# Optimization experiments

Measured on AMD Instinct MI355X. Metric: run time of the kernel, lower is better.

## Reference

```python
import jax, jax.numpy as jnp
import numpy as np

D_MODEL = 1024
STATE_DIM = 128


def setup_inputs() -> dict:
    key = jax.random.key(0)
    ks = jax.random.split(key, 8)
    B, T, D, N = 8, 4096, D_MODEL, STATE_DIM
    u = jax.random.normal(ks[0], (B, T, D), dtype=jnp.float32)
    h0 = jnp.zeros((B, N), dtype=jnp.float32)
    log_A = jax.random.normal(ks[1], (N,), dtype=jnp.float32) * 0.1 - 1.0
    B_w = jax.random.normal(ks[2], (N, D), dtype=jnp.float32) / np.sqrt(D)
    B_b = jax.random.normal(ks[3], (N,), dtype=jnp.float32) * 0.01
    C_w = jax.random.normal(ks[4], (D, N), dtype=jnp.float32) / np.sqrt(N)
    C_b = jax.random.normal(ks[5], (D,), dtype=jnp.float32) * 0.01
    D_param = jnp.ones((D,), dtype=jnp.float32) * 0.1
    log_dt = jax.random.normal(ks[6], (N,), dtype=jnp.float32) * 0.1 - 2.0
    return {"u": u, "h0": h0, "log_A": log_A, "B_w": B_w, "B_b": B_b,
            "C_w": C_w, "C_b": C_b, "D_param": D_param, "log_dt": log_dt}


def reference(u, h0, log_A, B_w, B_b, C_w, C_b, D_param, log_dt):
    # u: [B, T, D], h0: [B, N]
    dt = jnp.minimum(jnp.exp(log_dt), 1.0)          # [N]
    A = -jnp.exp(log_A)                             # [N]
    A_bar = jnp.exp(A * dt)                         # [N]
    # B_bar * u, precomputed for all timesteps: [B, T, N]
    Bu = (jnp.einsum('btd,nd->btn', u, B_w) + B_b) * dt

    def step(h, bu_t):
        h = A_bar * h + bu_t                        # [B, N]
        return h, h

    # scan over time: Bu transposed to [T, B, N]
    _, hs = jax.lax.scan(step, h0, jnp.swapaxes(Bu, 0, 1))
    hs = jnp.swapaxes(hs, 0, 1)                     # [B, T, N]
    # y = C h + c_bias + D * u
    y = jnp.einsum('btn,dn->btd', hs, C_w) + C_b + D_param * u
    return y
```

## Files before the change

### kernel.cpp

```cpp
#include <hip/hip_runtime.h>

#define B_SZ 8
#define T_SZ 4096
#define D_SZ 1024
#define N_SZ 128
#define M_SZ (B_SZ*T_SZ)
#define C1 32
#define NC1 (T_SZ/C1)
#define C2 64
#define NC2 (T_SZ/C2)

typedef __attribute__((ext_vector_type(8))) __bf16 bf16x8;
typedef __attribute__((ext_vector_type(4))) float f32x4;
typedef __attribute__((ext_vector_type(4))) unsigned int u32x4;
typedef __attribute__((ext_vector_type(4))) float fvec4;

static __device__ __forceinline__ unsigned short f2bf(float f){
  union { float f; unsigned int u; } v; v.f = f;
  unsigned int r = v.u + 0x7fffu + ((v.u >> 16) & 1u);
  return (unsigned short)(r >> 16);
}

static __device__ __forceinline__ float bf2f(unsigned short s){
  union { unsigned int u; float f; } v; v.u = ((unsigned)s) << 16;
  return v.f;
}

static __device__ __forceinline__ void cp16(const void* g, void* l){
  __builtin_amdgcn_global_load_lds(
      (const __attribute__((address_space(1))) void*)g,
      (__attribute__((address_space(3))) void*)l, 16, 0, 0);
}

static __device__ __forceinline__ f32x4 zero4(){
  f32x4 v = {0.f, 0.f, 0.f, 0.f};
  return v;
}

static __device__ __forceinline__ bf16x8 pack8(fvec4 a, fvec4 b){
  bf16x8 v;
  v[0]=(__bf16)a.x; v[1]=(__bf16)a.y; v[2]=(__bf16)a.z; v[3]=(__bf16)a.w;
  v[4]=(__bf16)b.x; v[5]=(__bf16)b.y; v[6]=(__bf16)b.z; v[7]=(__bf16)b.w;
  return v;
}

__global__ __launch_bounds__(256) void k_conv(const float* __restrict__ Bw,
                                              const float* __restrict__ Cw,
                                              unsigned short* __restrict__ bw,
                                              unsigned short* __restrict__ cw){
  int t = blockIdx.x*256 + threadIdx.x;
  {
    int n = t >> 10, k = t & 1023;
    int c = k >> 6, kk = k & 63;
    unsigned byte = (unsigned)c*16384u + (unsigned)n*128u
                  + (unsigned)((kk*2) ^ ((n&7)<<4));
    bw[byte>>1] = f2bf(Bw[n*1024 + k]);
  }
  {
    int d = t >> 7, k = t & 127;
    int c = d >> 7, dd = d & 127;
    unsigned byte = (unsigned)c*32768u + (unsigned)dd*256u
                  + (unsigned)((k*2) ^ ((dd&15)<<4));
    cw[byte>>1] = f2bf(Cw[d*128 + k]);
  }
}

__global__ __launch_bounds__(256, 4) void k_gemm1c(const float* __restrict__ u,
                                                   const unsigned short* __restrict__ bw,
                                                   const float* __restrict__ Bb,
                                                   const float* __restrict__ logA,
                                                   const float* __restrict__ logdt,
                                                   unsigned short* __restrict__ Bu_bf,
                                                   float* __restrict__ carry){
  __shared__ __align__(16) char smem[20480];
  unsigned short* lA = (unsigned short*)smem;
  unsigned short* lB = (unsigned short*)(smem + 4096);
  float*          BuT = (float*)smem;
  const int tid  = threadIdx.x;
  const int lane = tid & 63;
  const int wave = tid >> 6;
  const int bc   = blockIdx.x;
  const int m0   = bc * 32;
  const int l15  = lane & 15;
  const int lhi  = lane >> 4;
  const int rt   = (wave & 1) * 16;
  const int ct0  = (wave >> 1) * 4;

  f32x4 acc[4];
  #pragma unroll
  for (int i=0;i<4;++i) acc[i] = zero4();

  for (int kc=0; kc<16; ++kc){
    #pragma unroll
    for (int rep=0; rep<4; ++rep){
      const char* g = (const char*)bw + kc*16384 + rep*4096 + tid*16;
      cp16(g, (char*)lB + rep*4096 + tid*16);
    }
    {
      int row = tid >> 3, ks = tid & 7;
      const float* src = u + (size_t)(m0+row)*1024 + kc*64 + ks*8;
      fvec4 f0 = *(const fvec4*)src;
      fvec4 f1 = *(const fvec4*)(src+4);
      unsigned byte = (unsigned)row*128u + (unsigned)((ks*16) ^ ((row&7)<<4));
      *(bf16x8*)((char*)lA + byte) = pack8(f0, f1);
    }
    __syncthreads();
    #pragma unroll
    for (int k0=0; k0<64; k0+=32){
      int arow = rt + l15;
      int ak = k0 + lhi*8;
      bf16x8 af = *(const bf16x8*)((const char*)lA + arow*128 + ((ak*2) ^ ((arow&7)<<4)));
      #pragma unroll
      for (int j=0;j<4;++j){
        int bn = (ct0+j)*16 + l15;
        bf16x8 bfv = *(const bf16x8*)((const char*)lB + bn*128 + ((ak*2) ^ ((bn&7)<<4)));
        acc[j] = __builtin_amdgcn_mfma_f32_16x16x32_bf16(af, bfv, acc[j], 0, 0, 0);
      }
    }
    __builtin_amdgcn_s_barrier();
    __builtin_amdgcn_sched_barrier(0);
  }

  #pragma unroll
  for (int j=0;j<4;++j){
    int n = (ct0+j)*16 + l15;
    float dt = fminf(__expf(logdt[n]), 1.f);
    float bb = Bb[n];
    #pragma unroll
    for (int r=0;r<4;++r){
      int ml = rt + lhi*4 + r;
      BuT[ml*128 + n] = (acc[j][r] + bb) * dt;
    }
  }
  __syncthreads();

  #pragma unroll
  for (int i=0;i<2;++i){
    int q = i*256 + tid;
    const float* s = BuT + q*8;
    fvec4 a = *(const fvec4*)s;
    fvec4 b = *(const fvec4*)(s+4);
    u32x4 p;
    p.x = (unsigned)f2bf(a.x) | ((unsigned)f2bf(a.y)<<16);
    p.y = (unsigned)f2bf(a.z) | ((unsigned)f2bf(a.w)<<16);
    p.z = (unsigned)f2bf(b.x) | ((unsigned)f2bf(b.y)<<16);
    p.w = (unsigned)f2bf(b.z) | ((unsigned)f2bf(b.w)<<16);
    *(u32x4*)((char*)Bu_bf + (size_t)bc*8192 + (size_t)q*16) = p;
  }

  if (tid < 128){
    int n = tid;
    float dt = fminf(__expf(logdt[n]), 1.f);
    float Ab = __expf(-__expf(logA[n]) * dt);
    float h = 0.f;
    #pragma unroll 8
    for (int j=0;j<C1;++j) h = fmaf(Ab, h, BuT[j*128 + n]);
    carry[(size_t)bc*128 + n] = h;
  }
}

__global__ __launch_bounds__(256) void k_gemm2s(const unsigned short* __restrict__ Bu_bf,
                                                const float* __restrict__ carry,
                                                const unsigned short* __restrict__ cw,
                                                const float* __restrict__ u,
                                                const float* __restrict__ h0,
                                                const float* __restrict__ Cb,
                                                const float* __restrict__ Dp,
                                                const float* __restrict__ logA,
                                                const float* __restrict__ logdt,
                                                float* __restrict__ y){
  __shared__ __align__(16) unsigned short BuT[64*128];
  __shared__ __align__(16) unsigned short hsT[64*128];
  __shared__ __align__(16) unsigned short cwT[128*128];
  const int tid = threadIdx.x, lane = tid & 63, wave = tid >> 6;
  const int bc = blockIdx.x;
  const int m0 = bc * 64;
  const int l15 = lane & 15, lhi = lane >> 4;

  #pragma unroll
  for (int i=0;i<4;++i){
    int off = i*4096 + tid*16;
    cp16((const char*)Bu_bf + (size_t)bc*16384 + off, (char*)BuT + off);
  }
  #pragma unroll
  for (int i=0;i<8;++i){
    int off = i*4096 + tid*16;
    cp16((const char*)cw + off, (char*)cwT + off);
  }

  float hreg = 0.f, Ab = 0.f;
  if (tid < 128){
    int n = tid;
    int b = bc >> 6;
    int c32 = (bc & 63) * 2;
    float dt = fminf(__expf(logdt[n]), 1.f);
    float Ad = -__expf(logA[n]) * dt;
    Ab = __expf(Ad);
    float AL = __expf(Ad * (float)C1);
    float h = h0[b*128 + n];
    const float* cp = carry + (size_t)b*NC1*128 + n;
    for (int g=0; g<8; ++g){
      if (g*16 >= c32) break;
      float cbuf[16];
      #pragma unroll
      for (int i=0;i<16;++i) cbuf[i] = cp[(size_t)(g*16+i)*128];
      #pragma unroll
      for (int i=0;i<16;++i){
        int idx = g*16 + i;
        h = (idx < c32) ? fmaf(AL, h, cbuf[i]) : h;
      }
    }
    hreg = h;
  }
  __syncthreads();

  if (tid < 128){
    int n = tid;
    float h = hreg;
    #pragma unroll 8
    for (int j=0;j<C2;++j){
      h = fmaf(Ab, h, bf2f(BuT[j*128 + n]));
      unsigned byte = (unsigned)j*256u + (unsigned)((n*2) ^ ((j&15)<<4));
      *(unsigned short*)((char*)hsT + byte) = f2bf(h);
    }
  }
  __syncthreads();

  for (int d=0; d<8; ++d){
    f32x4 acc[8];
    #pragma unroll
    for (int i=0;i<8;++i) acc[i] = zero4();

    #pragma unroll
    for (int k0=0;k0<128;k0+=32){
      int arow = wave*16 + l15;
      int ak = k0 + lhi*8;
      bf16x8 af = *(const bf16x8*)((const char*)hsT + arow*256 + ((ak*2) ^ ((arow&15)<<4)));
      #pragma unroll
      for (int ct=0;ct<8;++ct){
        int dn = ct*16 + l15;
        bf16x8 bfv = *(const bf16x8*)((const char*)cwT + dn*256 + ((ak*2) ^ ((dn&15)<<4)));
        acc[ct] = __builtin_amdgcn_mfma_f32_16x16x32_bf16(af, bfv, acc[ct], 0, 0, 0);
      }
    }
    __builtin_amdgcn_s_barrier();
    __builtin_amdgcn_sched_barrier(0);

    if (d < 7){
      #pragma unroll
      for (int i=0;i<8;++i){
        int off = (wave*8 + i)*1024 + lane*16;
        cp16((const char*)cw + (size_t)(d+1)*32768 + off, (char*)cwT + off);
      }
    }

    const int d0 = d*128;
    #pragma unroll
    for (int ct=0;ct<8;++ct){
      int dc = d0 + ct*16 + l15;
      float cb = Cb[dc], dp = Dp[dc];
      #pragma unroll
      for (int r=0;r<4;++r){
        int m = m0 + wave*16 + lhi*4 + r;
        size_t off = (size_t)m*1024 + dc;
        y[off] = acc[ct][r] + cb + dp*u[off];
      }
    }
    asm volatile("s_waitcnt vmcnt(32)" ::: "memory");
    __builtin_amdgcn_s_barrier();
    __builtin_amdgcn_sched_barrier(0);
  }
}

extern "C" void kernel_launch(void* const* d_in, const int* in_sizes, int n_in,
                              void* d_out, int out_size, void* d_ws, size_t ws_size,
                              hipStream_t stream){
  (void)in_sizes; (void)n_in; (void)out_size; (void)ws_size;
  const float* u     = (const float*)d_in[0];
  const float* h0    = (const float*)d_in[1];
  const float* logA  = (const float*)d_in[2];
  const float* Bw    = (const float*)d_in[3];
  const float* Bb    = (const float*)d_in[4];
  const float* Cw    = (const float*)d_in[5];
  const float* Cb    = (const float*)d_in[6];
  const float* Dp    = (const float*)d_in[7];
  const float* logdt = (const float*)d_in[8];
  float* y = (float*)d_out;

  char* ws = (char*)d_ws;
  unsigned short* Bu_bf = (unsigned short*)(ws);
  float*          carry = (float*)(ws + 8388608);
  unsigned short* bw    = (unsigned short*)(ws + 8912896);
  unsigned short* cw    = (unsigned short*)(ws + 9175040);

  k_conv  <<<dim3(512),  dim3(256), 0, stream>>>(Bw, Cw, bw, cw);
  k_gemm1c<<<dim3(1024), dim3(256), 0, stream>>>(u, bw, Bb, logA, logdt, Bu_bf, carry);
  k_gemm2s<<<dim3(512),  dim3(256), 0, stream>>>(Bu_bf, carry, cw, u, h0, Cb, Dp,
                                                 logA, logdt, y);
}
```

Baseline: 86.66 us.

## Split scan from second GEMM and keep C weights in registers

Moves the carry propagation and intra-chunk scan into a separate k_scan kernel that writes bf16 hidden states, already laid out in the swizzled order, to workspace. The second GEMM is reorganised so each block owns one 128-wide D slice, holds that slice of C_w in registers for the whole block, and loops over 8 M-tiles with double-buffered async loads of the hidden states. This removes the serial scan from the GEMM kernel's critical path and stops each block from reloading all of C_w. In exchange it adds a kernel launch, an extra global round trip for hs, and heavy register use (launch_bounds 256,2).

```diff
diff --git a/kernel.cpp b/kernel.cpp
--- a/kernel.cpp
+++ b/kernel.cpp
@@ -117,8 +117,7 @@
         acc[j] = __builtin_amdgcn_mfma_f32_16x16x32_bf16(af, bfv, acc[j], 0, 0, 0);
       }
     }
-    __builtin_amdgcn_s_barrier();
-    __builtin_amdgcn_sched_barrier(0);
+    __syncthreads();
   }
 
   #pragma unroll
@@ -159,113 +158,126 @@
   }
 }
 
-__global__ __launch_bounds__(256) void k_gemm2s(const unsigned short* __restrict__ Bu_bf,
-                                                const float* __restrict__ carry,
-                                                const unsigned short* __restrict__ cw,
-                                                const float* __restrict__ u,
-                                                const float* __restrict__ h0,
-                                                const float* __restrict__ Cb,
-                                                const float* __restrict__ Dp,
-                                                const float* __restrict__ logA,
-                                                const float* __restrict__ logdt,
-                                                float* __restrict__ y){
-  __shared__ __align__(16) unsigned short BuT[64*128];
-  __shared__ __align__(16) unsigned short hsT[64*128];
-  __shared__ __align__(16) unsigned short cwT[128*128];
+__global__ __launch_bounds__(128) void k_scan(const unsigned short* __restrict__ Bu_bf,
+                                              const float* __restrict__ carry,
+                                              const float* __restrict__ h0,
+                                              const float* __restrict__ logA,
+                                              const float* __restrict__ logdt,
+                                              unsigned short* __restrict__ hs){
+  const int bc = blockIdx.x;
+  const int n  = threadIdx.x;
+  const int b  = bc >> 6;
+  const int c32 = (bc & 63) * 2;
+  float dt = fminf(__expf(logdt[n]), 1.f);
+  float Ad = -__expf(logA[n]) * dt;
+  float Ab = __expf(Ad);
+  float AL = __expf(Ad * (float)C1);
+  float h = h0[b*128 + n];
+  const float* cp = carry + (size_t)b*NC1*128 + n;
+  for (int g=0; g<8; ++g){
+    if (g*16 >= c32) break;
+    float cbuf[16];
+    #pragma unroll
+    for (int i=0;i<16;++i) cbuf[i] = cp[(size_t)(g*16+i)*128];
+    #pragma unroll
+    for (int i=0;i<16;++i){
+      int idx = g*16 + i;
+      h = (idx < c32) ? fmaf(AL, h, cbuf[i]) : h;
+    }
+  }
+  const unsigned short* bp = Bu_bf + (size_t)bc*C2*128 + n;
+  char* hbase = (char*)hs + (size_t)bc*16384;
+  #pragma unroll 8
+  for (int j=0;j<C2;++j){
+    h = fmaf(Ab, h, bf2f(bp[(size_t)j*128]));
+    unsigned byte = (unsigned)j*256u + (unsigned)((n*2) ^ ((j&15)<<4));
+    *(unsigned short*)(hbase + byte) = f2bf(h);
+  }
+}
+
+__global__ __launch_bounds__(256, 2) void k_gemm2(const unsigned short* __restrict__ hs,
+                                                  const unsigned short* __restrict__ cw,
+                                                  const float* __restrict__ u,
+                                                  const float* __restrict__ Cb,
+                                                  const float* __restrict__ Dp,
+                                                  float* __restrict__ y){
+  __shared__ __align__(16) unsigned short hsA[2][64*128];
   const int tid = threadIdx.x, lane = tid & 63, wave = tid >> 6;
-  const int bc = blockIdx.x;
-  const int m0 = bc * 64;
+  const int bid = blockIdx.x;
+  const int mg = bid & 63;
+  const int d  = bid >> 6;
   const int l15 = lane & 15, lhi = lane >> 4;
+  const int d0 = d*128;
 
   #pragma unroll
   for (int i=0;i<4;++i){
     int off = i*4096 + tid*16;
-    cp16((const char*)Bu_bf + (size_t)bc*16384 + off, (char*)BuT + off);
-  }
-  #pragma unroll
-  for (int i=0;i<8;++i){
-    int off = i*4096 + tid*16;
-    cp16((const char*)cw + off, (char*)cwT + off);
-  }
-
-  float hreg = 0.f, Ab = 0.f;
-  if (tid < 128){
-    int n = tid;
-    int b = bc >> 6;
-    int c32 = (bc & 63) * 2;
-    float dt = fminf(__expf(logdt[n]), 1.f);
-    float Ad = -__expf(logA[n]) * dt;
-    Ab = __expf(Ad);
-    float AL = __expf(Ad * (float)C1);
-    float h = h0[b*128 + n];
-    const float* cp = carry + (size_t)b*NC1*128 + n;
-    for (int g=0; g<8; ++g){
-      if (g*16 >= c32) break;
-      float cbuf[16];
-      #pragma unroll
-      for (int i=0;i<16;++i) cbuf[i] = cp[(size_t)(g*16+i)*128];
-      #pragma unroll
-      for (int i=0;i<16;++i){
-        int idx = g*16 + i;
-        h = (idx < c32) ? fmaf(AL, h, cbuf[i]) : h;
-      }
-    }
-    hreg = h;
-  }
-  __syncthreads();
-
-  if (tid < 128){
-    int n = tid;
-    float h = hreg;
-    #pragma unroll 8
-    for (int j=0;j<C2;++j){
-      h = fmaf(Ab, h, bf2f(BuT[j*128 + n]));
-      unsigned byte = (unsigned)j*256u + (unsigned)((n*2) ^ ((j&15)<<4));
-      *(unsigned short*)((char*)hsT + byte) = f2bf(h);
-    }
-  }
-  __syncthreads();
-
-  for (int d=0; d<8; ++d){
-    f32x4 acc[8];
-    #pragma unroll
-    for (int i=0;i<8;++i) acc[i] = zero4();
-
-    #pragma unroll
-    for (int k0=0;k0<128;k0+=32){
-      int arow = wave*16 + l15;
-      int ak = k0 + lhi*8;
-      bf16x8 af = *(const bf16x8*)((const char*)hsT + arow*256 + ((ak*2) ^ ((arow&15)<<4)));
+    cp16((const char*)hs + (size_t)(mg*8)*16384 + off, (char*)hsA[0] + off);
+  }
+
+  bf16x8 bfr[4][8];
+  {
+    const char* cwd = (const char*)cw + (size_t)d*32768;
+    #pragma unroll
+    for (int k0i=0;k0i<4;++k0i){
+      int ak = k0i*32 + lhi*8;
       #pragma unroll
       for (int ct=0;ct<8;++ct){
         int dn = ct*16 + l15;
-        bf16x8 bfv = *(const bf16x8*)((const char*)cwT + dn*256 + ((ak*2) ^ ((dn&15)<<4)));
-        acc[ct] = __builtin_amdgcn_mfma_f32_16x16x32_bf16(af, bfv, acc[ct], 0, 0, 0);
-      }
-    }
-    __builtin_amdgcn_s_barrier();
-    __builtin_amdgcn_sched_barrier(0);
-
-    if (d < 7){
-      #pragma unroll
-      for (int i=0;i<8;++i){
-        int off = (wave*8 + i)*1024 + lane*16;
-        cp16((const char*)cw + (size_t)(d+1)*32768 + off, (char*)cwT + off);
-      }
-    }
-
-    const int d0 = d*128;
+        bfr[k0i][ct] = *(const bf16x8*)(cwd + dn*256 + ((ak*2) ^ ((dn&15)<<4)));
+      }
+    }
+  }
+  float cbv[8], dpv[8];
+  #pragma unroll
+  for (int ct=0;ct<8;++ct){
+    int dc = d0 + ct*16 + l15;
+    cbv[ct] = Cb[dc]; dpv[ct] = Dp[dc];
+  }
+  __syncthreads();
+
+  for (int i=0;i<8;++i){
+    const int cur = i & 1;
+    const int m0 = mg*512 + i*64;
+
+    if (i < 7){
+      #pragma unroll
+      for (int r2=0;r2<4;++r2){
+        int off = r2*4096 + tid*16;
+        cp16((const char*)hs + (size_t)(mg*8+i+1)*16384 + off,
+             (char*)hsA[cur^1] + off);
+      }
+    }
+
+    f32x4 acc[8];
+    #pragma unroll
+    for (int j=0;j<8;++j) acc[j] = zero4();
+
+    {
+      const char* hb = (const char*)hsA[cur];
+      int arow = wave*16 + l15;
+      #pragma unroll
+      for (int k0i=0;k0i<4;++k0i){
+        int ak = k0i*32 + lhi*8;
+        bf16x8 af = *(const bf16x8*)(hb + arow*256 + ((ak*2) ^ ((arow&15)<<4)));
+        #pragma unroll
+        for (int ct=0;ct<8;++ct)
+          acc[ct] = __builtin_amdgcn_mfma_f32_16x16x32_bf16(af, bfr[k0i][ct],
+                                                            acc[ct], 0, 0, 0);
+      }
+    }
+
     #pragma unroll
     for (int ct=0;ct<8;++ct){
       int dc = d0 + ct*16 + l15;
-      float cb = Cb[dc], dp = Dp[dc];
       #pragma unroll
       for (int r=0;r<4;++r){
         int m = m0 + wave*16 + lhi*4 + r;
         size_t off = (size_t)m*1024 + dc;
-        y[off] = acc[ct][r] + cb + dp*u[off];
-      }
-    }
+        y[off] = acc[ct][r] + cbv[ct] + dpv[ct]*u[off];
+      }
+    }
+
     asm volatile("s_waitcnt vmcnt(32)" ::: "memory");
     __builtin_amdgcn_s_barrier();
     __builtin_amdgcn_sched_barrier(0);
@@ -292,9 +304,10 @@
   float*          carry = (float*)(ws + 8388608);
   unsigned short* bw    = (unsigned short*)(ws + 8912896);
   unsigned short* cw    = (unsigned short*)(ws + 9175040);
+  unsigned short* hsb   = (unsigned short*)(ws + 9437184);
 
   k_conv  <<<dim3(512),  dim3(256), 0, stream>>>(Bw, Cw, bw, cw);
   k_gemm1c<<<dim3(1024), dim3(256), 0, stream>>>(u, bw, Bb, logA, logdt, Bu_bf, carry);
-  k_gemm2s<<<dim3(512),  dim3(256), 0, stream>>>(Bu_bf, carry, cw, u, h0, Cb, Dp,
-                                                 logA, logdt, y);
-}
+  k_scan  <<<dim3(512),  dim3(128), 0, stream>>>(Bu_bf, carry, h0, logA, logdt, hsb);
+  k_gemm2 <<<dim3(512),  dim3(256), 0, stream>>>(hsb, cw, u, Cb, Dp, y);
+}
```

Measured after the change: 109.4 us. +26.2%, slower.
